# Optimization experiments

Hardware: AMD Instinct MI355X
Metric: run time of the kernel (lower is better)

The kernel has to match this reference:

```python
import jax, jax.numpy as jnp
import numpy as np

EPS = 1e-5

def instance_norm(x):
    # x: [B, C, H, W]; normalize over spatial dims per (b, c), no affine
    mean = jnp.mean(x, axis=(2, 3), keepdims=True)
    var = jnp.var(x, axis=(2, 3), keepdims=True)
    return (x - mean) * jax.lax.rsqrt(var + EPS)

def conv1x1(x, w, b):
    # x: [B, Cin, H, W], w: [Cout, Cin], b: [Cout]
    return jnp.einsum('bchw,oc->bohw', x, w) + b[None, :, None, None]

def setup_inputs() -> dict:
    key = jax.random.key(0)
    k1, k2, k3 = jax.random.split(key, 3)
    B, Cin, Cout, H, W = 16, 256, 256, 128, 128
    x = jax.random.normal(k1, (B, Cin, H, W), dtype=jnp.float32)
    # PyTorch Conv2d init: U(-s, s), s = 1/sqrt(fan_in) with fan_in = Cin*1*1
    s1 = 1.0 / np.sqrt(Cin)
    w1 = jax.random.uniform(k2, (Cout, Cin), jnp.float32, -s1, s1)
    b1 = jax.random.uniform(jax.random.fold_in(k2, 1), (Cout,), jnp.float32, -s1, s1)
    s2 = 1.0 / np.sqrt(Cout)
    w2 = jax.random.uniform(k3, (Cout, Cout), jnp.float32, -s2, s2)
    b2 = jax.random.uniform(jax.random.fold_in(k3, 1), (Cout,), jnp.float32, -s2, s2)
    return {"x": x, "w1": w1, "b1": b1, "w2": w2, "b2": b2}

def reference(x, w1, b1, w2, b2):
    h = jax.nn.relu(conv1x1(instance_norm(x), w1, b1))
    out = jax.nn.relu(conv1x1(instance_norm(h), w2, b2))
    return out
```

## Files before the change

kernel.cpp:

```cpp
#include <hip/hip_runtime.h>
#include <hip/hip_bf16.h>
#include <cstdint>
#include <cstddef>

#define DEVI __device__ __forceinline__

typedef unsigned short u16;
using frag_ab = __attribute__((ext_vector_type(8))) short;
using f32x4   = __attribute__((ext_vector_type(4))) float;

constexpr int HW = 16384;
constexpr int NC = 256;

DEVI u16 bf16bits(float f) {
    union { float f; uint32_t u; } cv; cv.f = f;
    uint32_t u = cv.u;
    u += 0x7fffu + ((u >> 16) & 1u);
    return (u16)(u >> 16);
}

DEVI void gload16(const void* g, void* l) {
    __builtin_amdgcn_global_load_lds(
        (const __attribute__((address_space(1))) uint32_t*)g,
        (__attribute__((address_space(3))) uint32_t*)l, 16, 0, 0);
}

DEVI frag_ab read_frag(const u16* slab, int row, int l4) {
    const int phys = (l4 ^ row ^ (row >> 2)) & 3;
    return *(const frag_ab*)((const char*)slab + row * 64 + phys * 16);
}

__global__ __launch_bounds__(256) void transpose_stats_kernel(
    const float* __restrict__ x, u16* __restrict__ xt,
    float* __restrict__ ps, float* __restrict__ pq)
{
    constexpr int PADW = 68;
    __shared__ __align__(16) u16 tile[64 * PADW];
    const int b = blockIdx.z, c0 = blockIdx.y * 64, p0 = blockIdx.x * 64;
    const int pblk = blockIdx.x;
    const int t = threadIdx.x;
    const int lane = t & 63, w = t >> 6;
    const int pq_ = lane & 15, cq = lane >> 4;
    const int quad = w * 4 + cq;
    const float* xb = x + ((size_t)b * NC + c0) * HW + p0;

    float va[4][4];
    float aS[4], aQ[4];
    #pragma unroll
    for (int j = 0; j < 4; ++j) {
        const float4 v = *(const float4*)(xb + (size_t)(quad * 4 + j) * HW + pq_ * 4);
        va[j][0] = v.x; va[j][1] = v.y; va[j][2] = v.z; va[j][3] = v.w;
        float s1 = v.x + v.y + v.z + v.w;
        float s2 = v.x*v.x + v.y*v.y + v.z*v.z + v.w*v.w;
        #pragma unroll
        for (int d = 1; d < 16; d <<= 1) {
            s1 += __shfl_xor(s1, d, 64);
            s2 += __shfl_xor(s2, d, 64);
        }
        aS[j] = s1; aQ[j] = s2;
    }
    if (pq_ == 0) {
        const float4 vs = {aS[0], aS[1], aS[2], aS[3]};
        const float4 vq = {aQ[0], aQ[1], aQ[2], aQ[3]};
        *(float4*)&ps[((size_t)b * 256 + pblk) * NC + c0 + quad * 4] = vs;
        *(float4*)&pq[((size_t)b * 256 + pblk) * NC + c0 + quad * 4] = vq;
    }
    #pragma unroll
    for (int i = 0; i < 4; ++i) {
        alignas(8) u16 pk[4];
        #pragma unroll
        for (int j = 0; j < 4; ++j) pk[j] = bf16bits(va[j][i]);
        *(uint2*)&tile[(pq_ * 4 + i) * PADW + quad * 4] = *(const uint2*)pk;
    }
    __syncthreads();
    const int pl = t >> 2, q = t & 3;
    u16* dst = xt + ((size_t)b * HW + p0 + pl) * NC + c0;
    #pragma unroll
    for (int s = 0; s < 2; ++s) {
        const int ch8 = q + s * 4;
        const uint2 lo = *(const uint2*)&tile[pl * PADW + ch8 * 8];
        const uint2 hi = *(const uint2*)&tile[pl * PADW + ch8 * 8 + 4];
        const uint4 o4 = {lo.x, lo.y, hi.x, hi.y};
        *(uint4*)(dst + ch8 * 8) = o4;
    }
}

__global__ __launch_bounds__(512) void fold_kernel(
    const float* __restrict__ w, const float* __restrict__ bias,
    const float* __restrict__ ps, const float* __restrict__ pq,
    u16* __restrict__ we, float* __restrict__ be)
{
    const int b = blockIdx.y, oc = blockIdx.x * 64;
    __shared__ float mu[NC], rs[NC];
    __shared__ float m1[2][NC], m2[2][NC];
    __shared__ __align__(16) float wt[64 * NC];
    const int t = threadIdx.x;
    {
        const int c = t & 255, half = t >> 8;
        float s1 = 0.f, s2 = 0.f;
        const float* pp = ps + (size_t)b * 256 * NC + (size_t)half * 128 * NC + c;
        const float* qq = pq + (size_t)b * 256 * NC + (size_t)half * 128 * NC + c;
        for (int i = 0; i < 128; ++i) {
            s1 += pp[(size_t)i * NC];
            s2 += qq[(size_t)i * NC];
        }
        m1[half][c] = s1; m2[half][c] = s2;
    }
    #pragma unroll
    for (int i = 0; i < 8; ++i)
        *(float4*)&wt[i*2048 + t*4] = *(const float4*)&w[(size_t)oc*NC + i*2048 + t*4];
    __syncthreads();
    if (t < NC) {
        const float s1 = m1[0][t] + m1[1][t];
        const float s2 = m2[0][t] + m2[1][t];
        const float m = s1 * (1.0f / HW);
        mu[t] = m;
        rs[t] = rsqrtf(s2 * (1.0f / HW) - m * m + 1e-5f);
    }
    __syncthreads();
    const int o = oc + (t >> 3), q = t & 7;
    const float* wrow = &wt[(t >> 3) * NC];
    u16* werow = we + ((size_t)b * NC + o) * NC;
    float bacc = 0.f;
    for (int cc = 0; cc < 4; ++cc) {
        alignas(16) u16 pk[8];
        #pragma unroll
        for (int jj = 0; jj < 8; ++jj) {
            const int c = q*32 + cc*8 + jj;
            const float wv = wrow[c];
            bacc -= wv * mu[c] * rs[c];
            pk[jj] = bf16bits(wv * rs[c]);
        }
        *(uint4*)(werow + q*32 + cc*8) = *(const uint4*)pk;
    }
    bacc += __shfl_xor(bacc, 1, 64);
    bacc += __shfl_xor(bacc, 2, 64);
    bacc += __shfl_xor(bacc, 4, 64);
    if (q == 0) be[b*NC + o] = bias[o] + bacc;
}

template<int STAGE>
__global__ __launch_bounds__(256, 2) void gemm_kernel(
    const u16* __restrict__ pixM,
    const u16* __restrict__ wMat,
    const float* __restrict__ biasE,
    u16* __restrict__ outB,
    float* __restrict__ outF,
    float* __restrict__ hps, float* __restrict__ hpq)
{
    __shared__ __align__(16) u16 ldsP[2][16384];

    const int b = blockIdx.x >> 6;
    const int g = blockIdx.x & 63;
    const int tid = threadIdx.x;
    const int lane = tid & 63, wid = tid >> 6;
    const int l15 = lane & 15, l4 = lane >> 4;

    const u16* gW = wMat + (size_t)b * NC * NC;

    const int rin  = lane >> 2;
    const int prow = wid * 16 + rin;
    const int psl  = ((lane & 3) ^ prow ^ (prow >> 2)) & 3;

    auto stageP = [&](int i, int buf) {
        const u16* gPt = pixM + ((size_t)b * HW + (g + 64 * i) * 64) * NC;
        #pragma unroll
        for (int ks = 0; ks < 8; ++ks)
            gload16(gPt + (size_t)prow * NC + ks * 32 + psl * 8,
                    (char*)ldsP[buf] + ks * 4096 + wid * 1024);
    };

    frag_ab wf[8][4];
    {
        const u16* wb = gW + (size_t)(wid * 64 + l15) * NC + l4 * 8;
        #pragma unroll
        for (int ks = 0; ks < 8; ++ks)
            #pragma unroll
            for (int f = 0; f < 4; ++f)
                wf[ks][f] = *(const frag_ab*)(wb + (size_t)f * 16 * NC + ks * 32);
    }
    float4 vb[4]; float bm[4];
    if constexpr (STAGE == 1) {
        #pragma unroll
        for (int mi = 0; mi < 4; ++mi)
            vb[mi] = *(const float4*)&biasE[b*NC + wid*64 + 16*mi + l4*4];
    } else {
        #pragma unroll
        for (int ni = 0; ni < 4; ++ni)
            bm[ni] = biasE[b*NC + wid*64 + 16*ni + l15];
    }

    stageP(0, 0);
    for (int i = 0; i < 4; ++i) {
        if (i == 0) {
            asm volatile("s_waitcnt vmcnt(0)" ::: "memory");
        } else if constexpr (STAGE == 1) {
            asm volatile("s_waitcnt vmcnt(24)" ::: "memory");
        } else {
            asm volatile("s_waitcnt vmcnt(16)" ::: "memory");
        }
        __builtin_amdgcn_s_barrier();
        if (i < 3) stageP(i + 1, (i + 1) & 1);
        asm volatile("" ::: "memory");

        f32x4 acc[4][4];
        #pragma unroll
        for (int mi = 0; mi < 4; ++mi)
            #pragma unroll
            for (int ni = 0; ni < 4; ++ni)
                acc[mi][ni] = (f32x4){0.f, 0.f, 0.f, 0.f};

        const u16* bufb = ldsP[i & 1];
        #pragma unroll
        for (int ks = 0; ks < 8; ++ks) {
            const u16* pslab = bufb + ks * 2048;
            frag_ab pf[4];
            #pragma unroll
            for (int f = 0; f < 4; ++f)
                pf[f] = read_frag(pslab, 16 * f + l15, l4);
            #pragma unroll
            for (int ni = 0; ni < 4; ++ni)
                #pragma unroll
                for (int mi = 0; mi < 4; ++mi) {
                    if constexpr (STAGE == 1)
                        acc[mi][ni] = __builtin_amdgcn_mfma_f32_16x16x32_bf16(wf[ks][mi], pf[ni], acc[mi][ni], 0, 0, 0);
                    else
                        acc[mi][ni] = __builtin_amdgcn_mfma_f32_16x16x32_bf16(pf[mi], wf[ks][ni], acc[mi][ni], 0, 0, 0);
                }
        }

        const int pblk = g + 64 * i;
        const int p0 = pblk * 64;
        if constexpr (STAGE == 1) {
            u16* htbase = outB + ((size_t)b * HW + p0) * NC + wid * 64;
            #pragma unroll
            for (int mi = 0; mi < 4; ++mi) {
                const float bx[4] = {vb[mi].x, vb[mi].y, vb[mi].z, vb[mi].w};
                float s1r[4] = {0.f,0.f,0.f,0.f}, s2r[4] = {0.f,0.f,0.f,0.f};
                #pragma unroll
                for (int ni = 0; ni < 4; ++ni) {
                    u16* rowp = htbase + (size_t)(16*ni + l15) * NC;
                    alignas(8) u16 pk[4];
                    #pragma unroll
                    for (int r = 0; r < 4; ++r) {
                        const float v = fmaxf(acc[mi][ni][r] + bx[r], 0.f);
                        s1r[r] += v; s2r[r] += v * v;
                        pk[r] = bf16bits(v);
                    }
                    *(uint2*)&rowp[16*mi + l4*4] = *(const uint2*)pk;
                }
                #pragma unroll
                for (int r = 0; r < 4; ++r) {
                    float a1 = s1r[r], a2 = s2r[r];
                    #pragma unroll
                    for (int d = 1; d < 16; d <<= 1) {
                        a1 += __shfl_xor(a1, d, 64);
                        a2 += __shfl_xor(a2, d, 64);
                    }
                    s1r[r] = a1; s2r[r] = a2;
                }
                if (l15 == 0) {
                    const int o = wid*64 + 16*mi + l4*4;
                    const float4 w1v = {s1r[0], s1r[1], s1r[2], s1r[3]};
                    const float4 w2v = {s2r[0], s2r[1], s2r[2], s2r[3]};
                    *(float4*)&hps[((size_t)b * 256 + pblk) * NC + o] = w1v;
                    *(float4*)&hpq[((size_t)b * 256 + pblk) * NC + o] = w2v;
                }
            }
        } else {
            #pragma unroll
            for (int ni = 0; ni < 4; ++ni) {
                const int o = wid*64 + 16*ni + l15;
                float* colp = outF + ((size_t)b * NC + o) * HW + p0;
                #pragma unroll
                for (int mi = 0; mi < 4; ++mi) {
                    const f32x4 v = {fmaxf(acc[mi][ni][0] + bm[ni], 0.f),
                                     fmaxf(acc[mi][ni][1] + bm[ni], 0.f),
                                     fmaxf(acc[mi][ni][2] + bm[ni], 0.f),
                                     fmaxf(acc[mi][ni][3] + bm[ni], 0.f)};
                    __builtin_nontemporal_store(v, (f32x4*)&colp[16*mi + l4*4]);
                }
            }
        }
    }
}

extern "C" void kernel_launch(void* const* d_in, const int* in_sizes, int n_in,
                              void* d_out, int out_size, void* d_ws, size_t ws_size,
                              hipStream_t stream)
{
    (void)in_sizes; (void)n_in; (void)out_size;
    const float* x  = (const float*)d_in[0];
    const float* w1 = (const float*)d_in[1];
    const float* b1 = (const float*)d_in[2];
    const float* w2 = (const float*)d_in[3];
    const float* b2 = (const float*)d_in[4];
    float* out = (float*)d_out;

    char* od = (char*)d_out;
    u16*   xt  = (u16*)od;
    float* xps = (float*)(od + 134217728);
    float* xpq = (float*)(od + 138412032);
    float* hps = (float*)(od + 142606336);
    float* hpq = (float*)(od + 146800640);

    char* ws = (char*)d_ws;
    const size_t NEED = 138444800;
    if (ws_size < NEED) return;
    u16*   ht  = (u16*)(ws);
    u16*   w1e = (u16*)(ws + 134217728);
    u16*   w2e = (u16*)(ws + 136314880);
    float* b1e = (float*)(ws + 138412032);
    float* b2e = (float*)(ws + 138428416);

    transpose_stats_kernel<<<dim3(HW/64, NC/64, 16), 256, 0, stream>>>(x, xt, xps, xpq);
    fold_kernel<<<dim3(4, 16), 512, 0, stream>>>(w1, b1, xps, xpq, w1e, b1e);
    gemm_kernel<1><<<dim3(1024), 256, 0, stream>>>(xt, w1e, b1e, ht, nullptr, hps, hpq);
    fold_kernel<<<dim3(4, 16), 512, 0, stream>>>(w2, b2, hps, hpq, w2e, b2e);
    gemm_kernel<2><<<dim3(1024), 256, 0, stream>>>(ht, w2e, b2e, nullptr, out, nullptr, nullptr);
}
```

Measured before the change: 286.1 us.

## Split stage-1 GEMM into 512-thread blocks with 32 output channels per wave

```diff
diff --git a/kernel.cpp b/kernel.cpp
--- a/kernel.cpp
+++ b/kernel.cpp
@@ -139,13 +139,11 @@
     if (q == 0) be[b*NC + o] = bias[o] + bacc;
 }
 
-template<int STAGE>
-__global__ __launch_bounds__(256, 2) void gemm_kernel(
+__global__ __launch_bounds__(512, 4) void gemm1_kernel(
     const u16* __restrict__ pixM,
     const u16* __restrict__ wMat,
     const float* __restrict__ biasE,
     u16* __restrict__ outB,
-    float* __restrict__ outF,
     float* __restrict__ hps, float* __restrict__ hpq)
 {
     __shared__ __align__(16) u16 ldsP[2][16384];
@@ -154,11 +152,126 @@
     const int g = blockIdx.x & 63;
     const int tid = threadIdx.x;
     const int lane = tid & 63, wid = tid >> 6;
-    const int l15 = lane & 15, l4 = lane >> 4;
+    const int l15 = lane & 15, l4 = lane >> 4, rin = lane >> 2;
 
     const u16* gW = wMat + (size_t)b * NC * NC;
-
-    const int rin  = lane >> 2;
+    const int obase = wid * 32;
+
+    auto stageP = [&](int i, int buf) {
+        const u16* gPt = pixM + ((size_t)b * HW + (g + 64 * i) * 64) * NC;
+        #pragma unroll
+        for (int q = 0; q < 4; ++q) {
+            const int j = q * 8 + wid, slice = j >> 2, rgrp = j & 3;
+            const int row = rgrp * 16 + rin;
+            const int sl = ((lane & 3) ^ row ^ (row >> 2)) & 3;
+            gload16(gPt + (size_t)row * NC + slice * 32 + sl * 8,
+                    (char*)ldsP[buf] + slice * 4096 + rgrp * 1024);
+        }
+    };
+
+    frag_ab wf[8][2];
+    {
+        const u16* wb = gW + (size_t)(obase + l15) * NC + l4 * 8;
+        #pragma unroll
+        for (int ks = 0; ks < 8; ++ks)
+            #pragma unroll
+            for (int f = 0; f < 2; ++f)
+                wf[ks][f] = *(const frag_ab*)(wb + (size_t)f * 16 * NC + ks * 32);
+    }
+    float4 vb[2];
+    #pragma unroll
+    for (int mi = 0; mi < 2; ++mi)
+        vb[mi] = *(const float4*)&biasE[b*NC + obase + 16*mi + l4*4];
+
+    stageP(0, 0);
+    for (int i = 0; i < 4; ++i) {
+        if (i == 0) asm volatile("s_waitcnt vmcnt(0)" ::: "memory");
+        else        asm volatile("s_waitcnt vmcnt(8)" ::: "memory");
+        __builtin_amdgcn_s_barrier();
+        if (i < 3) stageP(i + 1, (i + 1) & 1);
+        asm volatile("" ::: "memory");
+
+        f32x4 acc[2][4];
+        #pragma unroll
+        for (int mi = 0; mi < 2; ++mi)
+            #pragma unroll
+            for (int nj = 0; nj < 4; ++nj)
+                acc[mi][nj] = (f32x4){0.f, 0.f, 0.f, 0.f};
+
+        const u16* bufb = ldsP[i & 1];
+        #pragma unroll
+        for (int ks = 0; ks < 8; ++ks) {
+            const u16* pslab = bufb + ks * 2048;
+            #pragma unroll
+            for (int h = 0; h < 2; ++h) {
+                frag_ab pf[2];
+                #pragma unroll
+                for (int f = 0; f < 2; ++f)
+                    pf[f] = read_frag(pslab, 32*h + 16*f + l15, l4);
+                #pragma unroll
+                for (int f2 = 0; f2 < 2; ++f2)
+                    #pragma unroll
+                    for (int mi = 0; mi < 2; ++mi)
+                        acc[mi][2*h + f2] = __builtin_amdgcn_mfma_f32_16x16x32_bf16(
+                            wf[ks][mi], pf[f2], acc[mi][2*h + f2], 0, 0, 0);
+            }
+        }
+
+        const int pblk = g + 64 * i;
+        const int p0 = pblk * 64;
+        u16* htbase = outB + ((size_t)b * HW + p0) * NC + obase;
+        #pragma unroll
+        for (int mi = 0; mi < 2; ++mi) {
+            const float bx[4] = {vb[mi].x, vb[mi].y, vb[mi].z, vb[mi].w};
+            float s1r[4] = {0.f,0.f,0.f,0.f}, s2r[4] = {0.f,0.f,0.f,0.f};
+            #pragma unroll
+            for (int nj = 0; nj < 4; ++nj) {
+                u16* rowp = htbase + (size_t)(16*nj + l15) * NC;
+                alignas(8) u16 pk[4];
+                #pragma unroll
+                for (int r = 0; r < 4; ++r) {
+                    const float v = fmaxf(acc[mi][nj][r] + bx[r], 0.f);
+                    s1r[r] += v; s2r[r] += v * v;
+                    pk[r] = bf16bits(v);
+                }
+                *(uint2*)&rowp[16*mi + l4*4] = *(const uint2*)pk;
+            }
+            #pragma unroll
+            for (int r = 0; r < 4; ++r) {
+                float a1 = s1r[r], a2 = s2r[r];
+                #pragma unroll
+                for (int d = 1; d < 16; d <<= 1) {
+                    a1 += __shfl_xor(a1, d, 64);
+                    a2 += __shfl_xor(a2, d, 64);
+                }
+                s1r[r] = a1; s2r[r] = a2;
+            }
+            if (l15 == 0) {
+                const int o = obase + 16*mi + l4*4;
+                const float4 w1v = {s1r[0], s1r[1], s1r[2], s1r[3]};
+                const float4 w2v = {s2r[0], s2r[1], s2r[2], s2r[3]};
+                *(float4*)&hps[((size_t)b * 256 + pblk) * NC + o] = w1v;
+                *(float4*)&hpq[((size_t)b * 256 + pblk) * NC + o] = w2v;
+            }
+        }
+    }
+}
+
+__global__ __launch_bounds__(256, 2) void gemm2_kernel(
+    const u16* __restrict__ pixM,
+    const u16* __restrict__ wMat,
+    const float* __restrict__ biasE,
+    float* __restrict__ outF)
+{
+    __shared__ __align__(16) u16 ldsP[2][16384];
+
+    const int b = blockIdx.x >> 6;
+    const int g = blockIdx.x & 63;
+    const int tid = threadIdx.x;
+    const int lane = tid & 63, wid = tid >> 6;
+    const int l15 = lane & 15, l4 = lane >> 4, rin = lane >> 2;
+
+    const u16* gW = wMat + (size_t)b * NC * NC;
     const int prow = wid * 16 + rin;
     const int psl  = ((lane & 3) ^ prow ^ (prow >> 2)) & 3;
 
@@ -179,26 +292,15 @@
             for (int f = 0; f < 4; ++f)
                 wf[ks][f] = *(const frag_ab*)(wb + (size_t)f * 16 * NC + ks * 32);
     }
-    float4 vb[4]; float bm[4];
-    if constexpr (STAGE == 1) {
-        #pragma unroll
-        for (int mi = 0; mi < 4; ++mi)
-            vb[mi] = *(const float4*)&biasE[b*NC + wid*64 + 16*mi + l4*4];
-    } else {
-        #pragma unroll
-        for (int ni = 0; ni < 4; ++ni)
-            bm[ni] = biasE[b*NC + wid*64 + 16*ni + l15];
-    }
+    float bm[4];
+    #pragma unroll
+    for (int ni = 0; ni < 4; ++ni)
+        bm[ni] = biasE[b*NC + wid*64 + 16*ni + l15];
 
     stageP(0, 0);
     for (int i = 0; i < 4; ++i) {
-        if (i == 0) {
-            asm volatile("s_waitcnt vmcnt(0)" ::: "memory");
-        } else if constexpr (STAGE == 1) {
-            asm volatile("s_waitcnt vmcnt(24)" ::: "memory");
-        } else {
-            asm volatile("s_waitcnt vmcnt(16)" ::: "memory");
-        }
+        if (i == 0) asm volatile("s_waitcnt vmcnt(0)" ::: "memory");
+        else        asm volatile("s_waitcnt vmcnt(16)" ::: "memory");
         __builtin_amdgcn_s_barrier();
         if (i < 3) stageP(i + 1, (i + 1) & 1);
         asm volatile("" ::: "memory");
@@ -221,65 +323,23 @@
             #pragma unroll
             for (int ni = 0; ni < 4; ++ni)
                 #pragma unroll
-                for (int mi = 0; mi < 4; ++mi) {
-                    if constexpr (STAGE == 1)
-                        acc[mi][ni] = __builtin_amdgcn_mfma_f32_16x16x32_bf16(wf[ks][mi], pf[ni], acc[mi][ni], 0, 0, 0);
-                    else
-                        acc[mi][ni] = __builtin_amdgcn_mfma_f32_16x16x32_bf16(pf[mi], wf[ks][ni], acc[mi][ni], 0, 0, 0);
-                }
-        }
-
-        const int pblk = g + 64 * i;
-        const int p0 = pblk * 64;
-        if constexpr (STAGE == 1) {
-            u16* htbase = outB + ((size_t)b * HW + p0) * NC + wid * 64;
+                for (int mi = 0; mi < 4; ++mi)
+                    acc[mi][ni] = __builtin_amdgcn_mfma_f32_16x16x32_bf16(
+                        pf[mi], wf[ks][ni], acc[mi][ni], 0, 0, 0);
+        }
+
+        const int p0 = (g + 64 * i) * 64;
+        #pragma unroll
+        for (int ni = 0; ni < 4; ++ni) {
+            const int o = wid*64 + 16*ni + l15;
+            float* colp = outF + ((size_t)b * NC + o) * HW + p0;
             #pragma unroll
             for (int mi = 0; mi < 4; ++mi) {
-                const float bx[4] = {vb[mi].x, vb[mi].y, vb[mi].z, vb[mi].w};
-                float s1r[4] = {0.f,0.f,0.f,0.f}, s2r[4] = {0.f,0.f,0.f,0.f};
-                #pragma unroll
-                for (int ni = 0; ni < 4; ++ni) {
-                    u16* rowp = htbase + (size_t)(16*ni + l15) * NC;
-                    alignas(8) u16 pk[4];
-                    #pragma unroll
-                    for (int r = 0; r < 4; ++r) {
-                        const float v = fmaxf(acc[mi][ni][r] + bx[r], 0.f);
-                        s1r[r] += v; s2r[r] += v * v;
-                        pk[r] = bf16bits(v);
-                    }
-                    *(uint2*)&rowp[16*mi + l4*4] = *(const uint2*)pk;
-                }
-                #pragma unroll
-                for (int r = 0; r < 4; ++r) {
-                    float a1 = s1r[r], a2 = s2r[r];
-                    #pragma unroll
-                    for (int d = 1; d < 16; d <<= 1) {
-                        a1 += __shfl_xor(a1, d, 64);
-                        a2 += __shfl_xor(a2, d, 64);
-                    }
-                    s1r[r] = a1; s2r[r] = a2;
-                }
-                if (l15 == 0) {
-                    const int o = wid*64 + 16*mi + l4*4;
-                    const float4 w1v = {s1r[0], s1r[1], s1r[2], s1r[3]};
-                    const float4 w2v = {s2r[0], s2r[1], s2r[2], s2r[3]};
-                    *(float4*)&hps[((size_t)b * 256 + pblk) * NC + o] = w1v;
-                    *(float4*)&hpq[((size_t)b * 256 + pblk) * NC + o] = w2v;
-                }
-            }
-        } else {
-            #pragma unroll
-            for (int ni = 0; ni < 4; ++ni) {
-                const int o = wid*64 + 16*ni + l15;
-                float* colp = outF + ((size_t)b * NC + o) * HW + p0;
-                #pragma unroll
-                for (int mi = 0; mi < 4; ++mi) {
-                    const f32x4 v = {fmaxf(acc[mi][ni][0] + bm[ni], 0.f),
-                                     fmaxf(acc[mi][ni][1] + bm[ni], 0.f),
-                                     fmaxf(acc[mi][ni][2] + bm[ni], 0.f),
-                                     fmaxf(acc[mi][ni][3] + bm[ni], 0.f)};
-                    __builtin_nontemporal_store(v, (f32x4*)&colp[16*mi + l4*4]);
-                }
+                const f32x4 v = {fmaxf(acc[mi][ni][0] + bm[ni], 0.f),
+                                 fmaxf(acc[mi][ni][1] + bm[ni], 0.f),
+                                 fmaxf(acc[mi][ni][2] + bm[ni], 0.f),
+                                 fmaxf(acc[mi][ni][3] + bm[ni], 0.f)};
+                __builtin_nontemporal_store(v, (f32x4*)&colp[16*mi + l4*4]);
             }
         }
     }
@@ -315,7 +375,7 @@
 
     transpose_stats_kernel<<<dim3(HW/64, NC/64, 16), 256, 0, stream>>>(x, xt, xps, xpq);
     fold_kernel<<<dim3(4, 16), 512, 0, stream>>>(w1, b1, xps, xpq, w1e, b1e);
-    gemm_kernel<1><<<dim3(1024), 256, 0, stream>>>(xt, w1e, b1e, ht, nullptr, hps, hpq);
+    gemm1_kernel<<<dim3(1024), 512, 0, stream>>>(xt, w1e, b1e, ht, hps, hpq);
     fold_kernel<<<dim3(4, 16), 512, 0, stream>>>(w2, b2, hps, hpq, w2e, b2e);
-    gemm_kernel<2><<<dim3(1024), 256, 0, stream>>>(ht, w2e, b2e, nullptr, out, nullptr, nullptr);
-}
+    gemm2_kernel<<<dim3(1024), 256, 0, stream>>>(ht, w2e, b2e, out);
+}
```

Measured after the change: 308.9 us. 1.08x slower.
